# Kernel tuning notes

Hardware: AMD Instinct MI355X
Metric: run time of the kernel (lower is better)

## Reference

```python
import jax, jax.numpy as jnp
import numpy as np

ALPHA = 0.8  # LeakyReLU negative slope
OUT_DIM = 128
EDGE_DIM = 64


def setup_inputs() -> dict:
    key = jax.random.key(0)
    ks = jax.random.split(key, 6)
    N, NS, IN, OUT, ED = 25000, 32, 128, OUT_DIM, EDGE_DIM
    return {
        "input": jax.random.normal(ks[0], (N, IN), jnp.float32),
        "neigh_feat": jax.random.normal(ks[1], (N * NS, IN), jnp.float32),
        "edge_emb": jax.random.normal(ks[2], (N * NS, ED), jnp.float32),
        "mask": jnp.zeros((N,), jnp.int32),  # unused by forward, kept for signature fidelity
        "W": jax.random.normal(ks[3], (IN, OUT), jnp.float32) * 0.1,
        "W2": jax.random.normal(ks[4], (IN, OUT), jnp.float32) * 0.1,
        "a": jax.random.normal(ks[5], (2 * OUT + ED, 1), jnp.float32) * 0.1,
    }


def reference(input, neigh_feat, edge_emb, mask, W, W2, a):
    N = input.shape[0]
    ns = neigh_feat.shape[0] // N
    out_dim = W.shape[1]
    ed = edge_emb.shape[1]

    x = input @ W                                   # [N, out]
    neighs = (neigh_feat @ W2).reshape(N, ns, out_dim)  # [N, ns, out]
    edge = edge_emb.reshape(N, ns, ed)              # [N, ns, ed]

    # a_input @ a decomposed: avoid materializing the repeated/concatenated tensor.
    a_x = a[:out_dim, 0]
    a_n = a[out_dim:2 * out_dim, 0]
    a_e = a[2 * out_dim:, 0]
    scores = (x @ a_x)[:, None] + neighs @ a_n + edge @ a_e  # [N, ns]
    e = jnp.where(scores > 0, scores, ALPHA * scores)        # LeakyReLU(alpha)

    attention = jax.nn.softmax(e, axis=1)           # softmax over neighbors
    # dropout p=0.0 (eval) -> identity

    h_prime = jnp.einsum("ns,nsd->nd", attention, neighs)  # [N, out]
    output = jnp.concatenate([x, h_prime], axis=1)          # concat_node
    e_agg = jnp.einsum("ns,nse->ne", attention, edge)       # concat_edge
    output = jnp.concatenate([output, e_agg], axis=1)       # [N, 2*out+ed]
    return jax.nn.elu(output)
```

## Files before the change

kernel.cpp:

```cpp
#include <hip/hip_runtime.h>
#include <hip/hip_bf16.h>
#include <math.h>

typedef __bf16 bf16_t;
typedef __attribute__((ext_vector_type(8))) __bf16 bf16x8;
typedef __attribute__((ext_vector_type(4))) float f32x4;
typedef __attribute__((ext_vector_type(2))) float f32x2;

#define NB 8

__global__ __launch_bounds__(256) void pack_weights_kernel(
    const float* __restrict__ W, const float* __restrict__ W2,
    const float* __restrict__ a,
    bf16_t* __restrict__ Wp, bf16_t* __restrict__ W2p,
    float* __restrict__ w2an) {
  int idx = blockIdx.x * 256 + threadIdx.x;
  int j  = idx & 7;
  int l  = (idx >> 3) & 63;
  int nt = (idx >> 9) & 7;
  int kt = idx >> 12;
  int k   = kt * 32 + (l >> 4) * 8 + j;
  int col = nt * 16 + (l & 15);
  Wp[idx]  = (bf16_t)W[k * 128 + col];
  W2p[idx] = (bf16_t)W2[k * 128 + col];
  if (blockIdx.x == 0 && threadIdx.x < 128) {
    const float* r = W2 + threadIdx.x * 128;
    float s = 0.f;
    for (int c = 0; c < 128; ++c) s += r[c] * a[128 + c];
    w2an[threadIdx.x] = s;
  }
}

__global__ __launch_bounds__(256) void gemm_kernel(
    const float* __restrict__ src, const bf16_t* __restrict__ Wpk,
    const float* __restrict__ a,
    float* __restrict__ out, float* __restrict__ sxv, int col_off, int N) {
  __shared__ __align__(16) bf16_t As[32 * 128];
  __shared__ float sp2[2][32];
  const int t  = threadIdx.x;
  const int rb = blockIdx.x * 32;
  const int w = t >> 6, l = t & 63;

  for (int c = t; c < 512; c += 256) {
    int row = c >> 4;
    int kc  = (c & 15) * 8;
    int grow = rb + row;
    float v[8];
    if (grow < N) {
      const f32x4* p = (const f32x4*)(src + (size_t)grow * 128 + kc);
      f32x4 v0 = p[0], v1 = p[1];
      v[0]=v0[0]; v[1]=v0[1]; v[2]=v0[2]; v[3]=v0[3];
      v[4]=v1[0]; v[5]=v1[1]; v[6]=v1[2]; v[7]=v1[3];
    } else {
      for (int j = 0; j < 8; ++j) v[j] = 0.f;
    }
    bf16x8 b;
    for (int j = 0; j < 8; ++j) b[j] = (bf16_t)v[j];
    *(bf16x8*)(&As[row * 128 + (kc ^ ((row & 7) << 3))]) = b;
  }
  __syncthreads();

  const int mt = w & 1;
  const int ntg = (w >> 1) * 4;
  const int arow = mt * 16 + (l & 15);

  f32x4 acc[4] = {};
#pragma unroll
  for (int kt = 0; kt < 4; ++kt) {
    bf16x8 af = *(const bf16x8*)(&As[arow * 128 + ((kt * 32 + (l >> 4) * 8) ^ ((arow & 7) << 3))]);
#pragma unroll
    for (int i = 0; i < 4; ++i) {
      bf16x8 bfv = *(const bf16x8*)(&Wpk[((kt * 8 + (ntg + i)) * 64 + l) * 8]);
      acc[i] = __builtin_amdgcn_mfma_f32_16x16x32_bf16(af, bfv, acc[i], 0, 0, 0);
    }
  }

  if (sxv) {
    float ax[4];
#pragma unroll
    for (int i = 0; i < 4; ++i) ax[i] = a[(ntg + i) * 16 + (l & 15)];
#pragma unroll
    for (int j = 0; j < 4; ++j) {
      float p = acc[0][j]*ax[0] + acc[1][j]*ax[1] + acc[2][j]*ax[2] + acc[3][j]*ax[3];
      p += __shfl_xor(p, 1); p += __shfl_xor(p, 2);
      p += __shfl_xor(p, 4); p += __shfl_xor(p, 8);
      if ((l & 15) == 0) sp2[w >> 1][mt * 16 + (l >> 4) * 4 + j] = p;
    }
    __syncthreads();
    if (t < 32) {
      int gr = rb + t;
      if (gr < N) sxv[gr] = sp2[0][t] + sp2[1][t];
    }
  }

#pragma unroll
  for (int i = 0; i < 4; ++i) {
    int col = (ntg + i) * 16 + (l & 15);
#pragma unroll
    for (int j = 0; j < 4; ++j) {
      int row = mt * 16 + (l >> 4) * 4 + j;
      int gr = rb + row;
      if (gr < N) {
        float v = acc[i][j];
        out[(size_t)gr * 320 + col_off + col] = v > 0.f ? v : __expf(v) - 1.f;
      }
    }
  }
}

__global__ __launch_bounds__(256) void node_kernel(
    const float* __restrict__ neigh_feat, const float* __restrict__ edge_emb,
    const float* __restrict__ a, const float* __restrict__ w2an,
    const float* __restrict__ sxv, float* __restrict__ aggbuf,
    float* __restrict__ out) {
  const int t = threadIdx.x;
  const int w = t >> 6, l = t & 63;
  const int n0 = blockIdx.x * NB;

  __shared__ __align__(16) bf16_t As[2][32 * 128];
  __shared__ __align__(16) bf16_t Eb[2][32 * 64];
  __shared__ float srow[2][32];
  __shared__ float se[2][32];

  const int es = t >> 3, sub = t & 7;
  const int r0 = t >> 4, kc0 = (t & 15) * 8;
  const int swz = (r0 & 7) << 3;

  const f32x4 ae0 = *(const f32x4*)(a + 256 + sub * 8);
  const f32x4 ae1 = *(const f32x4*)(a + 256 + sub * 8 + 4);
  const f32x4 wn0 = *(const f32x4*)(w2an + kc0);
  const f32x4 wn1 = *(const f32x4*)(w2an + kc0 + 4);

  f32x4 nv0, nv1, nv2, nv3, ev0, ev1;
#define ISSUE(node_) do {                                                   \
    const float* nf_ = neigh_feat + (size_t)(node_) * 4096;                 \
    nv0 = *(const f32x4*)(nf_ + r0 * 128 + kc0);                            \
    nv1 = *(const f32x4*)(nf_ + r0 * 128 + kc0 + 4);                        \
    nv2 = *(const f32x4*)(nf_ + (r0 + 16) * 128 + kc0);                     \
    nv3 = *(const f32x4*)(nf_ + (r0 + 16) * 128 + kc0 + 4);                 \
    const float* ee_ = edge_emb + (size_t)(node_) * 2048 + es * 64 + sub * 8; \
    ev0 = *(const f32x4*)(ee_);                                             \
    ev1 = *(const f32x4*)(ee_ + 4);                                         \
  } while (0)

  ISSUE(n0);
  int buf = 0;

#pragma unroll 1
  for (int k = 0; k < NB; ++k) {
    const int node = n0 + k;

    {
      float pe = ev0[0]*ae0[0] + ev0[1]*ae0[1] + ev0[2]*ae0[2] + ev0[3]*ae0[3]
               + ev1[0]*ae1[0] + ev1[1]*ae1[1] + ev1[2]*ae1[2] + ev1[3]*ae1[3];
      pe += __shfl_xor(pe, 1); pe += __shfl_xor(pe, 2); pe += __shfl_xor(pe, 4);
      if (sub == 0) se[buf][es] = pe;

      float p0 = nv0[0]*wn0[0] + nv0[1]*wn0[1] + nv0[2]*wn0[2] + nv0[3]*wn0[3]
               + nv1[0]*wn1[0] + nv1[1]*wn1[1] + nv1[2]*wn1[2] + nv1[3]*wn1[3];
      float p1 = nv2[0]*wn0[0] + nv2[1]*wn0[1] + nv2[2]*wn0[2] + nv2[3]*wn0[3]
               + nv3[0]*wn1[0] + nv3[1]*wn1[1] + nv3[2]*wn1[2] + nv3[3]*wn1[3];
      p0 += __shfl_xor(p0, 1); p0 += __shfl_xor(p0, 2);
      p0 += __shfl_xor(p0, 4); p0 += __shfl_xor(p0, 8);
      p1 += __shfl_xor(p1, 1); p1 += __shfl_xor(p1, 2);
      p1 += __shfl_xor(p1, 4); p1 += __shfl_xor(p1, 8);
      if ((l & 15) == 0) { srow[buf][r0] = p0; srow[buf][r0 + 16] = p1; }

      bf16x8 b0, b1, ebv;
#pragma unroll
      for (int j = 0; j < 4; ++j) {
        b0[j] = (bf16_t)nv0[j]; b0[j+4] = (bf16_t)nv1[j];
        b1[j] = (bf16_t)nv2[j]; b1[j+4] = (bf16_t)nv3[j];
        ebv[j] = (bf16_t)ev0[j]; ebv[j+4] = (bf16_t)ev1[j];
      }
      *(bf16x8*)(&As[buf][r0 * 128 + (kc0 ^ swz)])        = b0;
      *(bf16x8*)(&As[buf][(r0 + 16) * 128 + (kc0 ^ swz)]) = b1;
      *(bf16x8*)(&Eb[buf][es * 64 + ((sub ^ (es & 7)) * 8)]) = ebv;
    }
    __syncthreads();

    if (k + 1 < NB) ISSUE(node + 1);

    float av;
    {
      const float sx = sxv[node];
      int s = l & 31;
      float e = srow[buf][s] + se[buf][s] + sx;
      e = e > 0.f ? e : 0.8f * e;
      float m = e;
      m = fmaxf(m, __shfl_xor(m, 1));
      m = fmaxf(m, __shfl_xor(m, 2));
      m = fmaxf(m, __shfl_xor(m, 4));
      m = fmaxf(m, __shfl_xor(m, 8));
      m = fmaxf(m, __shfl_xor(m, 16));
      float pe2 = __expf(e - m);
      float s2 = pe2;
      s2 += __shfl_xor(s2, 1);
      s2 += __shfl_xor(s2, 2);
      s2 += __shfl_xor(s2, 4);
      s2 += __shfl_xor(s2, 8);
      s2 += __shfl_xor(s2, 16);
      av = pe2 / s2;
    }

    if (w == 0) {
      const int g = l >> 2;
      const int boff = (l & 3) * 4;
      const char* base = (const char*)As[buf];
      float a0 = 0.f, a1 = 0.f;
#pragma unroll
      for (int s = 0; s < 32; ++s) {
        unsigned u = *(const unsigned*)(base + s * 256 + ((g ^ (s & 7)) * 16) + boff);
        float as = __shfl(av, s);
        a0 = fmaf(as, __uint_as_float(u << 16), a0);
        a1 = fmaf(as, __uint_as_float(u & 0xffff0000u), a1);
      }
      f32x2 st = {a0, a1};
      *(f32x2*)(aggbuf + (size_t)node * 128 + 2 * l) = st;
    } else if (w == 1 && l < 32) {
      const int g = l >> 2;
      const int boff = (l & 3) * 4;
      const char* base = (const char*)Eb[buf];
      float a0 = 0.f, a1 = 0.f;
#pragma unroll
      for (int s = 0; s < 32; ++s) {
        unsigned u = *(const unsigned*)(base + s * 128 + ((g ^ (s & 7)) * 16) + boff);
        float as = __shfl(av, s);
        a0 = fmaf(as, __uint_as_float(u << 16), a0);
        a1 = fmaf(as, __uint_as_float(u & 0xffff0000u), a1);
      }
      a0 = a0 > 0.f ? a0 : __expf(a0) - 1.f;
      a1 = a1 > 0.f ? a1 : __expf(a1) - 1.f;
      f32x2 st = {a0, a1};
      *(f32x2*)(out + (size_t)node * 320 + 256 + 2 * l) = st;
    }
    buf ^= 1;
  }
#undef ISSUE
}

extern "C" void kernel_launch(void* const* d_in, const int* in_sizes, int n_in,
                              void* d_out, int out_size, void* d_ws, size_t ws_size,
                              hipStream_t stream) {
  const float* input = (const float*)d_in[0];
  const float* neigh = (const float*)d_in[1];
  const float* edge  = (const float*)d_in[2];
  const float* W     = (const float*)d_in[4];
  const float* W2    = (const float*)d_in[5];
  const float* a     = (const float*)d_in[6];
  float* out = (float*)d_out;

  const int N = in_sizes[0] / 128;

  bf16_t* W2p  = (bf16_t*)d_ws;
  bf16_t* Wp   = W2p + 16384;
  float*  w2an = (float*)((char*)d_ws + 65536);
  float*  sxv  = (float*)((char*)d_ws + 66560);
  float*  agg  = (float*)((char*)d_ws + 262144);

  pack_weights_kernel<<<64, 256, 0, stream>>>(W, W2, a, Wp, W2p, w2an);
  gemm_kernel<<<(N + 31) / 32, 256, 0, stream>>>(input, Wp, a, out, sxv, 0, N);
  node_kernel<<<N / NB, 256, 0, stream>>>(neigh, edge, a, w2an, sxv, agg, out);
  gemm_kernel<<<(N + 31) / 32, 256, 0, stream>>>(agg, W2p, a, out, nullptr, 128, N);
}
```

Baseline: 164.4 us.

## Deepen node_kernel prefetch to two nodes and fuse score reductions per row

The node kernel now keeps two register sets (A/B) and issues loads two nodes ahead instead of one, so more global memory traffic is in flight while the current node is processed. The thread-to-data mapping changes so that each group of 8 threads owns one neighbor row, covering both its neighbor features and its edge embedding. This merges the neighbor and edge score dot products into a single 3-step shuffle reduction and removes the separate se buffer. Output stores become nontemporal to avoid polluting the cache. The cost is higher register pressure from the doubled prefetch buffers, which may reduce occupancy.

```diff
diff --git a/kernel.cpp b/kernel.cpp
--- a/kernel.cpp
+++ b/kernel.cpp
@@ -102,7 +102,8 @@
       int gr = rb + row;
       if (gr < N) {
         float v = acc[i][j];
-        out[(size_t)gr * 320 + col_off + col] = v > 0.f ? v : __expf(v) - 1.f;
+        v = v > 0.f ? v : __expf(v) - 1.f;
+        __builtin_nontemporal_store(v, &out[(size_t)gr * 320 + col_off + col]);
       }
     }
   }
@@ -116,126 +117,122 @@
   const int t = threadIdx.x;
   const int w = t >> 6, l = t & 63;
   const int n0 = blockIdx.x * NB;
+  const int r = t >> 3, sub = t & 7;
+  const int c0 = sub * 16;
 
   __shared__ __align__(16) bf16_t As[2][32 * 128];
   __shared__ __align__(16) bf16_t Eb[2][32 * 64];
   __shared__ float srow[2][32];
-  __shared__ float se[2][32];
-
-  const int es = t >> 3, sub = t & 7;
-  const int r0 = t >> 4, kc0 = (t & 15) * 8;
-  const int swz = (r0 & 7) << 3;
-
+
+  const f32x4 wn0 = *(const f32x4*)(w2an + c0);
+  const f32x4 wn1 = *(const f32x4*)(w2an + c0 + 4);
+  const f32x4 wn2 = *(const f32x4*)(w2an + c0 + 8);
+  const f32x4 wn3 = *(const f32x4*)(w2an + c0 + 12);
   const f32x4 ae0 = *(const f32x4*)(a + 256 + sub * 8);
   const f32x4 ae1 = *(const f32x4*)(a + 256 + sub * 8 + 4);
-  const f32x4 wn0 = *(const f32x4*)(w2an + kc0);
-  const f32x4 wn1 = *(const f32x4*)(w2an + kc0 + 4);
-
-  f32x4 nv0, nv1, nv2, nv3, ev0, ev1;
-#define ISSUE(node_) do {                                                   \
-    const float* nf_ = neigh_feat + (size_t)(node_) * 4096;                 \
-    nv0 = *(const f32x4*)(nf_ + r0 * 128 + kc0);                            \
-    nv1 = *(const f32x4*)(nf_ + r0 * 128 + kc0 + 4);                        \
-    nv2 = *(const f32x4*)(nf_ + (r0 + 16) * 128 + kc0);                     \
-    nv3 = *(const f32x4*)(nf_ + (r0 + 16) * 128 + kc0 + 4);                 \
-    const float* ee_ = edge_emb + (size_t)(node_) * 2048 + es * 64 + sub * 8; \
-    ev0 = *(const f32x4*)(ee_);                                             \
-    ev1 = *(const f32x4*)(ee_ + 4);                                         \
+
+  const int wrA = r * 128 + (((sub * 2) ^ (r & 7)) * 8);
+  const int wrB = r * 128 + ((((sub * 2) + 1) ^ (r & 7)) * 8);
+  const int wrE = r * 64 + ((sub ^ (r & 7)) * 8);
+
+  f32x4 nA0, nA1, nA2, nA3, eA0, eA1;
+  f32x4 nB0, nB1, nB2, nB3, eB0, eB1;
+
+#define ISSUE(P, node_) do {                                               \
+    const float* nf_ = neigh_feat + (size_t)(node_) * 4096 + r * 128 + c0; \
+    n##P##0 = *(const f32x4*)(nf_);                                        \
+    n##P##1 = *(const f32x4*)(nf_ + 4);                                    \
+    n##P##2 = *(const f32x4*)(nf_ + 8);                                    \
+    n##P##3 = *(const f32x4*)(nf_ + 12);                                   \
+    const float* ee_ = edge_emb + (size_t)(node_) * 2048 + r * 64 + sub * 8; \
+    e##P##0 = *(const f32x4*)(ee_);                                        \
+    e##P##1 = *(const f32x4*)(ee_ + 4);                                    \
   } while (0)
 
-  ISSUE(n0);
-  int buf = 0;
+#define BODY(P, b, kk) do {                                                 \
+    const int node = n0 + (kk);                                             \
+    {                                                                       \
+      float p = n##P##0[0]*wn0[0] + n##P##0[1]*wn0[1] + n##P##0[2]*wn0[2] + n##P##0[3]*wn0[3] \
+              + n##P##1[0]*wn1[0] + n##P##1[1]*wn1[1] + n##P##1[2]*wn1[2] + n##P##1[3]*wn1[3] \
+              + n##P##2[0]*wn2[0] + n##P##2[1]*wn2[1] + n##P##2[2]*wn2[2] + n##P##2[3]*wn2[3] \
+              + n##P##3[0]*wn3[0] + n##P##3[1]*wn3[1] + n##P##3[2]*wn3[2] + n##P##3[3]*wn3[3] \
+              + e##P##0[0]*ae0[0] + e##P##0[1]*ae0[1] + e##P##0[2]*ae0[2] + e##P##0[3]*ae0[3] \
+              + e##P##1[0]*ae1[0] + e##P##1[1]*ae1[1] + e##P##1[2]*ae1[2] + e##P##1[3]*ae1[3]; \
+      p += __shfl_xor(p, 1); p += __shfl_xor(p, 2); p += __shfl_xor(p, 4);  \
+      if (sub == 0) srow[b][r] = p;                                         \
+      bf16x8 x0, x1, xe;                                                    \
+      _Pragma("unroll")                                                     \
+      for (int j = 0; j < 4; ++j) {                                         \
+        x0[j] = (bf16_t)n##P##0[j]; x0[j+4] = (bf16_t)n##P##1[j];           \
+        x1[j] = (bf16_t)n##P##2[j]; x1[j+4] = (bf16_t)n##P##3[j];           \
+        xe[j] = (bf16_t)e##P##0[j]; xe[j+4] = (bf16_t)e##P##1[j];           \
+      }                                                                     \
+      *(bf16x8*)(&As[b][wrA]) = x0;                                         \
+      *(bf16x8*)(&As[b][wrB]) = x1;                                         \
+      *(bf16x8*)(&Eb[b][wrE]) = xe;                                         \
+    }                                                                       \
+    if ((kk) + 2 < NB) ISSUE(P, node + 2);                                  \
+    __syncthreads();                                                        \
+    float av;                                                               \
+    {                                                                       \
+      const float sx = sxv[node];                                           \
+      float e = srow[b][l & 31] + sx;                                       \
+      e = e > 0.f ? e : 0.8f * e;                                           \
+      float m = e;                                                          \
+      m = fmaxf(m, __shfl_xor(m, 1));                                       \
+      m = fmaxf(m, __shfl_xor(m, 2));                                       \
+      m = fmaxf(m, __shfl_xor(m, 4));                                       \
+      m = fmaxf(m, __shfl_xor(m, 8));                                       \
+      m = fmaxf(m, __shfl_xor(m, 16));                                      \
+      float pe = __expf(e - m);                                             \
+      float s2 = pe;                                                        \
+      s2 += __shfl_xor(s2, 1);                                              \
+      s2 += __shfl_xor(s2, 2);                                              \
+      s2 += __shfl_xor(s2, 4);                                              \
+      s2 += __shfl_xor(s2, 8);                                              \
+      s2 += __shfl_xor(s2, 16);                                             \
+      av = pe / s2;                                                         \
+    }                                                                       \
+    if (w == 0) {                                                           \
+      const int gg = l >> 2, boff = (l & 3) * 4;                            \
+      const char* base = (const char*)As[b];                                \
+      float a0 = 0.f, a1 = 0.f;                                             \
+      _Pragma("unroll")                                                     \
+      for (int s = 0; s < 32; ++s) {                                        \
+        unsigned u = *(const unsigned*)(base + s * 256 + ((gg ^ (s & 7)) * 16) + boff); \
+        float as = __shfl(av, s);                                           \
+        a0 = fmaf(as, __uint_as_float(u << 16), a0);                        \
+        a1 = fmaf(as, __uint_as_float(u & 0xffff0000u), a1);                \
+      }                                                                     \
+      f32x2 st = {a0, a1};                                                  \
+      *(f32x2*)(aggbuf + (size_t)node * 128 + 2 * l) = st;                  \
+    } else if (w == 1 && l < 32) {                                          \
+      const int gg = l >> 2, boff = (l & 3) * 4;                            \
+      const char* base = (const char*)Eb[b];                                \
+      float a0 = 0.f, a1 = 0.f;                                             \
+      _Pragma("unroll")                                                     \
+      for (int s = 0; s < 32; ++s) {                                        \
+        unsigned u = *(const unsigned*)(base + s * 128 + ((gg ^ (s & 7)) * 16) + boff); \
+        float as = __shfl(av, s);                                           \
+        a0 = fmaf(as, __uint_as_float(u << 16), a0);                        \
+        a1 = fmaf(as, __uint_as_float(u & 0xffff0000u), a1);                \
+      }                                                                     \
+      a0 = a0 > 0.f ? a0 : __expf(a0) - 1.f;                                \
+      a1 = a1 > 0.f ? a1 : __expf(a1) - 1.f;                                \
+      f32x2 st = {a0, a1};                                                  \
+      __builtin_nontemporal_store(st, (f32x2*)(out + (size_t)node * 320 + 256 + 2 * l)); \
+    }                                                                       \
+  } while (0)
+
+  ISSUE(A, n0);
+  ISSUE(B, n0 + 1);
 
 #pragma unroll 1
-  for (int k = 0; k < NB; ++k) {
-    const int node = n0 + k;
-
-    {
-      float pe = ev0[0]*ae0[0] + ev0[1]*ae0[1] + ev0[2]*ae0[2] + ev0[3]*ae0[3]
-               + ev1[0]*ae1[0] + ev1[1]*ae1[1] + ev1[2]*ae1[2] + ev1[3]*ae1[3];
-      pe += __shfl_xor(pe, 1); pe += __shfl_xor(pe, 2); pe += __shfl_xor(pe, 4);
-      if (sub == 0) se[buf][es] = pe;
-
-      float p0 = nv0[0]*wn0[0] + nv0[1]*wn0[1] + nv0[2]*wn0[2] + nv0[3]*wn0[3]
-               + nv1[0]*wn1[0] + nv1[1]*wn1[1] + nv1[2]*wn1[2] + nv1[3]*wn1[3];
-      float p1 = nv2[0]*wn0[0] + nv2[1]*wn0[1] + nv2[2]*wn0[2] + nv2[3]*wn0[3]
-               + nv3[0]*wn1[0] + nv3[1]*wn1[1] + nv3[2]*wn1[2] + nv3[3]*wn1[3];
-      p0 += __shfl_xor(p0, 1); p0 += __shfl_xor(p0, 2);
-      p0 += __shfl_xor(p0, 4); p0 += __shfl_xor(p0, 8);
-      p1 += __shfl_xor(p1, 1); p1 += __shfl_xor(p1, 2);
-      p1 += __shfl_xor(p1, 4); p1 += __shfl_xor(p1, 8);
-      if ((l & 15) == 0) { srow[buf][r0] = p0; srow[buf][r0 + 16] = p1; }
-
-      bf16x8 b0, b1, ebv;
-#pragma unroll
-      for (int j = 0; j < 4; ++j) {
-        b0[j] = (bf16_t)nv0[j]; b0[j+4] = (bf16_t)nv1[j];
-        b1[j] = (bf16_t)nv2[j]; b1[j+4] = (bf16_t)nv3[j];
-        ebv[j] = (bf16_t)ev0[j]; ebv[j+4] = (bf16_t)ev1[j];
-      }
-      *(bf16x8*)(&As[buf][r0 * 128 + (kc0 ^ swz)])        = b0;
-      *(bf16x8*)(&As[buf][(r0 + 16) * 128 + (kc0 ^ swz)]) = b1;
-      *(bf16x8*)(&Eb[buf][es * 64 + ((sub ^ (es & 7)) * 8)]) = ebv;
-    }
-    __syncthreads();
-
-    if (k + 1 < NB) ISSUE(node + 1);
-
-    float av;
-    {
-      const float sx = sxv[node];
-      int s = l & 31;
-      float e = srow[buf][s] + se[buf][s] + sx;
-      e = e > 0.f ? e : 0.8f * e;
-      float m = e;
-      m = fmaxf(m, __shfl_xor(m, 1));
-      m = fmaxf(m, __shfl_xor(m, 2));
-      m = fmaxf(m, __shfl_xor(m, 4));
-      m = fmaxf(m, __shfl_xor(m, 8));
-      m = fmaxf(m, __shfl_xor(m, 16));
-      float pe2 = __expf(e - m);
-      float s2 = pe2;
-      s2 += __shfl_xor(s2, 1);
-      s2 += __shfl_xor(s2, 2);
-      s2 += __shfl_xor(s2, 4);
-      s2 += __shfl_xor(s2, 8);
-      s2 += __shfl_xor(s2, 16);
-      av = pe2 / s2;
-    }
-
-    if (w == 0) {
-      const int g = l >> 2;
-      const int boff = (l & 3) * 4;
-      const char* base = (const char*)As[buf];
-      float a0 = 0.f, a1 = 0.f;
-#pragma unroll
-      for (int s = 0; s < 32; ++s) {
-        unsigned u = *(const unsigned*)(base + s * 256 + ((g ^ (s & 7)) * 16) + boff);
-        float as = __shfl(av, s);
-        a0 = fmaf(as, __uint_as_float(u << 16), a0);
-        a1 = fmaf(as, __uint_as_float(u & 0xffff0000u), a1);
-      }
-      f32x2 st = {a0, a1};
-      *(f32x2*)(aggbuf + (size_t)node * 128 + 2 * l) = st;
-    } else if (w == 1 && l < 32) {
-      const int g = l >> 2;
-      const int boff = (l & 3) * 4;
-      const char* base = (const char*)Eb[buf];
-      float a0 = 0.f, a1 = 0.f;
-#pragma unroll
-      for (int s = 0; s < 32; ++s) {
-        unsigned u = *(const unsigned*)(base + s * 128 + ((g ^ (s & 7)) * 16) + boff);
-        float as = __shfl(av, s);
-        a0 = fmaf(as, __uint_as_float(u << 16), a0);
-        a1 = fmaf(as, __uint_as_float(u & 0xffff0000u), a1);
-      }
-      a0 = a0 > 0.f ? a0 : __expf(a0) - 1.f;
-      a1 = a1 > 0.f ? a1 : __expf(a1) - 1.f;
-      f32x2 st = {a0, a1};
-      *(f32x2*)(out + (size_t)node * 320 + 256 + 2 * l) = st;
-    }
-    buf ^= 1;
-  }
+  for (int k = 0; k < NB; k += 2) {
+    BODY(A, 0, k);
+    BODY(B, 1, k + 1);
+  }
+#undef BODY
 #undef ISSUE
 }
 
```

Result: no change. 164.9 us (+0.3%).
